# Optimization experiments

Hardware: AMD Instinct MI355X
Metric: run time of the kernel (lower is better)

The kernel has to match this reference:

```python
import jax, jax.numpy as jnp
import numpy as np
import math

D_MODEL = 1024
NUM_HEADS = 16
D_K = D_MODEL // NUM_HEADS
SEQ_LEN = 2048
THETA = 10000.0


def _rope_tables(seq_len, d_k, theta):
    # inv_freq over even dims, angles repeated-interleaved to full d_k
    inv_freq = theta ** (-jnp.arange(0, d_k, 2, dtype=jnp.float32) / d_k)  # [d_k/2]
    pos = jnp.arange(seq_len, dtype=jnp.float32)                          # [s]
    angles = pos[:, None] * inv_freq[None, :]                             # [s, d_k/2]
    angles = jnp.repeat(angles, 2, axis=-1)                               # [s, d_k]
    return jnp.cos(angles), jnp.sin(angles)


def _rotate_half(x):
    # interleaved pairs: (x0,x1,x2,x3,...) -> (-x1,x0,-x3,x2,...)
    x_even = x[..., ::2]
    x_odd = x[..., 1::2]
    return jnp.stack([-x_odd, x_even], axis=-1).reshape(x.shape)


def _apply_rope(x, cos, sin):
    # x: [b, h, s, d_k]; cos/sin: [s, d_k]
    return x * cos + _rotate_half(x) * sin


def setup_inputs() -> dict:
    key = jax.random.key(0)
    ks = jax.random.split(key, 5)
    scale = 1.0 / math.sqrt(D_MODEL)
    X = jax.random.normal(ks[0], (2, SEQ_LEN, D_MODEL), dtype=jnp.float32)
    Wq = jax.random.normal(ks[1], (D_MODEL, D_MODEL), dtype=jnp.float32) * scale
    Wk = jax.random.normal(ks[2], (D_MODEL, D_MODEL), dtype=jnp.float32) * scale
    Wv = jax.random.normal(ks[3], (D_MODEL, D_MODEL), dtype=jnp.float32) * scale
    Wo = jax.random.normal(ks[4], (D_MODEL, D_MODEL), dtype=jnp.float32) * scale
    return {"X": X, "Wq": Wq, "Wk": Wk, "Wv": Wv, "Wo": Wo}


def reference(X, Wq, Wk, Wv, Wo):
    b, s, _ = X.shape
    h, dk = NUM_HEADS, D_K

    def proj(W):
        return (X @ W.T).reshape(b, s, h, dk).transpose(0, 2, 1, 3)  # [b,h,s,dk]

    q, k, v = proj(Wq), proj(Wk), proj(Wv)

    cos, sin = _rope_tables(s, dk, THETA)
    q = _apply_rope(q, cos, sin)
    k = _apply_rope(k, cos, sin)

    scores = jnp.einsum('bhid,bhjd->bhij', q, k) / math.sqrt(dk)
    causal = jnp.tril(jnp.ones((s, s), dtype=bool))
    scores = jnp.where(causal[None, None], scores, -jnp.inf)
    probs = jax.nn.softmax(scores, axis=-1)
    attended = jnp.einsum('bhij,bhjd->bhid', probs, v)               # [b,h,s,dk]

    out = attended.transpose(0, 2, 1, 3).reshape(b, s, h * dk)
    return out @ Wo.T
```

## Files before the change

kernel.cpp:

```cpp
#include <hip/hip_runtime.h>
#include <stdint.h>

#define D_MODEL 1024
#define NUM_HEADS 16
#define DK 64
#define SEQ 2048
#define BATCH 2
#define MROWS (BATCH * SEQ)
#define LOG2E 1.4426950408889634f
#define FIXM 14.0f

typedef short bf16x8 __attribute__((ext_vector_type(8)));
typedef float f32x4 __attribute__((ext_vector_type(4)));

__device__ __forceinline__ unsigned short f2bf(float f) {
    unsigned int u = __float_as_uint(f);
    u = (u + 0x7fffu + ((u >> 16) & 1u)) >> 16;
    return (unsigned short)u;
}
__device__ __forceinline__ unsigned short f2bf_trunc(float f) {
    return (unsigned short)(__float_as_uint(f) >> 16);
}
__device__ __forceinline__ float bf2f(unsigned short h) {
    return __uint_as_float(((unsigned int)h) << 16);
}
__device__ __forceinline__ void async16(const void* g, void* l) {
    __builtin_amdgcn_global_load_lds(
        (const __attribute__((address_space(1))) void*)g,
        (__attribute__((address_space(3))) void*)l, 16, 0, 0);
}
#define SWZ64(row, b) ((((row) * 8) + ((b) ^ ((row) & 7))) * 8)

__global__ void cast_all(const float4* __restrict__ X, const float4* __restrict__ Wq,
                         const float4* __restrict__ Wk, const float4* __restrict__ Wv,
                         const float4* __restrict__ Wo, ushort4* __restrict__ Xb,
                         ushort4* __restrict__ Wqkvb, ushort4* __restrict__ Wob) {
    int i = blockIdx.x * blockDim.x + threadIdx.x;
    const float4* src;
    ushort4* dst;
    int off;
    if (i < 1048576) { src = X; dst = Xb; off = i; }
    else if (i < 1310720) { src = Wq; dst = Wqkvb; off = i - 1048576; }
    else if (i < 1572864) { src = Wk; dst = Wqkvb + 262144; off = i - 1310720; }
    else if (i < 1835008) { src = Wv; dst = Wqkvb + 524288; off = i - 1572864; }
    else { src = Wo; dst = Wob; off = i - 1835008; }
    float4 v = src[off];
    ushort4 o;
    o.x = f2bf(v.x); o.y = f2bf(v.y); o.z = f2bf(v.z); o.w = f2bf(v.w);
    dst[off] = o;
}

template <int TN, int OUT_BF16>
__global__ __launch_bounds__(256) void gemm_tile(
    const unsigned short* __restrict__ A, const unsigned short* __restrict__ B,
    void* __restrict__ Cout, int M, int N, int K) {
    __shared__ unsigned short As[128 * 64];
    __shared__ unsigned short Bs[TN * 64];
    const int m0 = blockIdx.y * 128, n0 = blockIdx.x * TN;
    const int t = threadIdx.x;
    const int lane = t & 63, wave = t >> 6;
    const int mA = lane & 15, quad = lane >> 4;
    constexpr int MI = (TN == 128) ? 4 : 2;
    constexpr int NI = 4;
    const int wr = (TN == 128) ? (wave >> 1) * 64 : wave * 32;
    const int wc = (TN == 128) ? (wave & 1) * 64 : 0;

    f32x4 acc[MI][NI] = {};
    for (int k0 = 0; k0 < K; k0 += 64) {
#pragma unroll
        for (int i = 0; i < 4; ++i) {
            int ch = i * 256 + t;
            int r = ch >> 3, b = (ch & 7) ^ (r & 7);
            async16(A + (size_t)(m0 + r) * K + k0 + b * 8, (char*)As + ch * 16);
        }
#pragma unroll
        for (int i = 0; i < TN / 32; ++i) {
            int ch = i * 256 + t;
            int r = ch >> 3, b = (ch & 7) ^ (r & 7);
            async16(B + (size_t)(n0 + r) * K + k0 + b * 8, (char*)Bs + ch * 16);
        }
        __syncthreads();
#pragma unroll
        for (int kk = 0; kk < 2; ++kk) {
            bf16x8 af[MI], bfr[NI];
#pragma unroll
            for (int mi = 0; mi < MI; ++mi) {
                int rr = wr + mi * 16 + mA;
                af[mi] = *(const bf16x8*)&As[SWZ64(rr, kk * 4 + quad)];
            }
#pragma unroll
            for (int ni = 0; ni < NI; ++ni) {
                int rr = wc + ni * 16 + mA;
                bfr[ni] = *(const bf16x8*)&Bs[SWZ64(rr, kk * 4 + quad)];
            }
#pragma unroll
            for (int mi = 0; mi < MI; ++mi)
#pragma unroll
                for (int ni = 0; ni < NI; ++ni)
                    acc[mi][ni] = __builtin_amdgcn_mfma_f32_16x16x32_bf16(
                        af[mi], bfr[ni], acc[mi][ni], 0, 0, 0);
        }
        __syncthreads();
    }
#pragma unroll
    for (int mi = 0; mi < MI; ++mi)
#pragma unroll
        for (int ni = 0; ni < NI; ++ni)
#pragma unroll
            for (int r = 0; r < 4; ++r) {
                int gm = m0 + wr + mi * 16 + quad * 4 + r;
                int gn = n0 + wc + ni * 16 + mA;
                if (OUT_BF16)
                    ((unsigned short*)Cout)[(size_t)gm * N + gn] = f2bf(acc[mi][ni][r]);
                else
                    ((float*)Cout)[(size_t)gm * N + gn] = acc[mi][ni][r];
            }
}

__global__ __launch_bounds__(256) void rope_vt(const unsigned short* __restrict__ QKV,
                                               unsigned short* __restrict__ Qr,
                                               unsigned short* __restrict__ Kr,
                                               unsigned short* __restrict__ Vt) {
    __shared__ unsigned short T[64][80];
    const int bx = blockIdx.x;
    const int t = threadIdx.x;
    if (bx < 4096) {
        int tid = bx * 256 + t;
        int bs = tid >> 8;
        int p4 = tid & 255;
        int b = bs >> 11, spos = bs & 2047;
        int h = p4 >> 4, dd = (p4 & 15) * 4;
        float sn0, cs0, sn1, cs1;
        {
            float if0 = __expf(-(float)dd * (9.210340371976184f / 64.0f));
            float if1 = __expf(-(float)(dd + 2) * (9.210340371976184f / 64.0f));
            __sincosf((float)spos * if0, &sn0, &cs0);
            __sincosf((float)spos * if1, &sn1, &cs1);
        }
        size_t src = (size_t)bs * 3072 + h * 64 + dd;
        ushort4 qw = *(const ushort4*)&QKV[src];
        ushort4 kw = *(const ushort4*)&QKV[src + 1024];
        ushort4 qo_, ko_;
        float e = bf2f(qw.x), o = bf2f(qw.y);
        qo_.x = f2bf(e * cs0 - o * sn0); qo_.y = f2bf(o * cs0 + e * sn0);
        e = bf2f(qw.z); o = bf2f(qw.w);
        qo_.z = f2bf(e * cs1 - o * sn1); qo_.w = f2bf(o * cs1 + e * sn1);
        e = bf2f(kw.x); o = bf2f(kw.y);
        ko_.x = f2bf(e * cs0 - o * sn0); ko_.y = f2bf(o * cs0 + e * sn0);
        e = bf2f(kw.z); o = bf2f(kw.w);
        ko_.z = f2bf(e * cs1 - o * sn1); ko_.w = f2bf(o * cs1 + e * sn1);
        size_t qb = (((size_t)(b * NUM_HEADS + h) * SEQ + spos) * DK + dd);
        *(ushort4*)&Qr[qb] = qo_;
        *(ushort4*)&Kr[qb] = ko_;
    } else {
        int idx = bx - 4096;
        const int s0 = (idx & 31) * 64, bh = idx >> 5;
        const int b = bh >> 4, h = bh & 15;
#pragma unroll
        for (int i = 0; i < 2; ++i) {
            int ch = i * 256 + t;
            int row = ch >> 3, bc = ch & 7;
            *(int4*)&T[row][bc * 8] =
                *(const int4*)&QKV[(size_t)(b * SEQ + s0 + row) * 3072 + 2048 + h * 64 + bc * 8];
        }
        __syncthreads();
#pragma unroll
        for (int i = 0; i < 2; ++i) {
            int ch = i * 256 + t;
            int d = ch >> 3, sb = ch & 7;
            unsigned short tmp[8];
#pragma unroll
            for (int j = 0; j < 8; ++j) tmp[j] = T[sb * 8 + j][d];
            *(int4*)&Vt[(size_t)bh * DK * SEQ + (size_t)d * SEQ + s0 + sb * 8] = *(int4*)tmp;
        }
    }
}

__global__ __launch_bounds__(256, 4) void flash_attn6(
    const unsigned short* __restrict__ Qr, const unsigned short* __restrict__ Kr,
    const unsigned short* __restrict__ Vt, unsigned short* __restrict__ Att) {
    __shared__ unsigned short Ks[2][64 * 64];
    __shared__ unsigned short Vs[2][64 * 64];
    __shared__ unsigned short Ps[4][16 * 64];
    const int bh = blockIdx.x;
    const int qt = 31 - (int)blockIdx.y;
    const int t = threadIdx.x;
    const int lane = t & 63, wave = t >> 6;
    const int mA = lane & 15, quad = lane >> 4;
    const int qr0 = qt * 64 + wave * 16;
    const size_t qkbase = (size_t)bh * SEQ * DK;
    const unsigned short* Kg = Kr + qkbase;
    const unsigned short* Vg = Vt + (size_t)bh * DK * SEQ;

    bf16x8 aq[2];
#pragma unroll
    for (int c = 0; c < 2; ++c) {
        bf16x8 raw = *(const bf16x8*)&Qr[qkbase + (size_t)(qr0 + mA) * DK + c * 32 + quad * 8];
        bf16x8 s;
#pragma unroll
        for (int j = 0; j < 8; ++j)
            s[j] = (short)f2bf(bf2f((unsigned short)raw[j]) * (0.125f * LOG2E));
        aq[c] = s;
    }

    f32x4 accT[4] = {};
    float lsum[4] = {};

#pragma unroll
    for (int i = 0; i < 2; ++i) {
        int ch = i * 256 + t;
        int row = ch >> 3, sb = (ch & 7) ^ (row & 7);
        async16(Kg + (size_t)row * DK + sb * 8, (char*)Ks[0] + ch * 16);
        async16(Vg + (size_t)row * SEQ + sb * 8, (char*)Vs[0] + ch * 16);
    }

    for (int jt = 0; jt <= qt; ++jt) {
        __syncthreads();
        const int cur = jt & 1;
        if (jt < qt) {
            const int j1 = (jt + 1) * 64;
#pragma unroll
            for (int i = 0; i < 2; ++i) {
                int ch = i * 256 + t;
                int row = ch >> 3, sb = (ch & 7) ^ (row & 7);
                async16(Kg + (size_t)(j1 + row) * DK + sb * 8, (char*)Ks[cur ^ 1] + ch * 16);
                async16(Vg + (size_t)row * SEQ + j1 + sb * 8, (char*)Vs[cur ^ 1] + ch * 16);
            }
        }
        const int j0 = jt * 64;
        const unsigned short* Kt = Ks[cur];
        const unsigned short* Vtile = Vs[cur];
        unsigned short* Pw = Ps[wave];

        f32x4 sc[4] = {};
#pragma unroll
        for (int js = 0; js < 4; ++js) {
            int row = js * 16 + mA;
            bf16x8 b0 = *(const bf16x8*)&Kt[SWZ64(row, quad)];
            bf16x8 b1 = *(const bf16x8*)&Kt[SWZ64(row, quad + 4)];
            sc[js] = __builtin_amdgcn_mfma_f32_16x16x32_bf16(aq[0], b0, sc[js], 0, 0, 0);
            sc[js] = __builtin_amdgcn_mfma_f32_16x16x32_bf16(aq[1], b1, sc[js], 0, 0, 0);
        }
        if (jt == qt) {
#pragma unroll
            for (int js = 0; js < 4; ++js) {
                int gcol = j0 + js * 16 + mA;
#pragma unroll
                for (int r = 0; r < 4; ++r)
                    if (gcol > qr0 + quad * 4 + r) sc[js][r] = -1e30f;
            }
        }

#pragma unroll
        for (int js = 0; js < 4; ++js)
#pragma unroll
            for (int r = 0; r < 4; ++r) {
                float p = __builtin_amdgcn_exp2f(sc[js][r] - FIXM);
                lsum[r] += p;
                int q = quad * 4 + r;
                Pw[SWZ64(q, js * 2 + (mA >> 3)) + (mA & 7)] = f2bf_trunc(p);
            }
        bf16x8 ap0 = *(const bf16x8*)&Pw[SWZ64(mA, quad)];
        bf16x8 ap1 = *(const bf16x8*)&Pw[SWZ64(mA, quad + 4)];
#pragma unroll
        for (int tn = 0; tn < 4; ++tn) {
            int row = tn * 16 + mA;
            bf16x8 bv0 = *(const bf16x8*)&Vtile[SWZ64(row, quad)];
            bf16x8 bv1 = *(const bf16x8*)&Vtile[SWZ64(row, quad + 4)];
            accT[tn] = __builtin_amdgcn_mfma_f32_16x16x32_bf16(bv0, ap0, accT[tn], 0, 0, 0);
            accT[tn] = __builtin_amdgcn_mfma_f32_16x16x32_bf16(bv1, ap1, accT[tn], 0, 0, 0);
        }
    }

#pragma unroll
    for (int r = 0; r < 4; ++r)
#pragma unroll
        for (int off = 1; off < 16; off <<= 1)
            lsum[r] += __shfl_xor(lsum[r], off, 64);
    __syncthreads();
    float* LL = (float*)Ks;
    if (mA == 0)
#pragma unroll
        for (int r = 0; r < 4; ++r) LL[wave * 16 + quad * 4 + r] = lsum[r];
    __syncthreads();
    const float rl = 1.0f / LL[wave * 16 + mA];

    const int b = bh >> 4, h = bh & 15;
#pragma unroll
    for (int tn = 0; tn < 4; ++tn) {
        ushort4 o;
        o.x = f2bf(accT[tn][0] * rl);
        o.y = f2bf(accT[tn][1] * rl);
        o.z = f2bf(accT[tn][2] * rl);
        o.w = f2bf(accT[tn][3] * rl);
        *(ushort4*)&Att[(size_t)(b * SEQ + qr0 + mA) * D_MODEL + h * DK + tn * 16 + quad * 4] = o;
    }
}

extern "C" void kernel_launch(void* const* d_in, const int* in_sizes, int n_in,
                              void* d_out, int out_size, void* d_ws, size_t ws_size,
                              hipStream_t stream) {
    const float* X = (const float*)d_in[0];
    const float* Wq = (const float*)d_in[1];
    const float* Wk = (const float*)d_in[2];
    const float* Wv = (const float*)d_in[3];
    const float* Wo = (const float*)d_in[4];

    char* ws = (char*)d_ws;
    unsigned short* Xb     = (unsigned short*)(ws + 0);
    unsigned short* Wqkvb  = (unsigned short*)(ws + (8u << 20));
    unsigned short* Wob    = (unsigned short*)(ws + (14u << 20));
    unsigned short* QKVraw = (unsigned short*)(ws + (16u << 20));
    unsigned short* Kr     = (unsigned short*)(ws + (40u << 20));
    unsigned short* Vt     = (unsigned short*)(ws + (48u << 20));
    unsigned short* Qr     = Xb;
    unsigned short* Att    = QKVraw;

    cast_all<<<8192, 256, 0, stream>>>((const float4*)X, (const float4*)Wq,
                                       (const float4*)Wk, (const float4*)Wv,
                                       (const float4*)Wo, (ushort4*)Xb,
                                       (ushort4*)Wqkvb, (ushort4*)Wob);

    gemm_tile<128, 1><<<dim3(3072 / 128, MROWS / 128), 256, 0, stream>>>(
        Xb, Wqkvb, QKVraw, MROWS, 3072, D_MODEL);

    rope_vt<<<4096 + 1024, 256, 0, stream>>>(QKVraw, Qr, Kr, Vt);

    flash_attn6<<<dim3(BATCH * NUM_HEADS, 32), 256, 0, stream>>>(Qr, Kr, Vt, Att);

    gemm_tile<64, 0><<<dim3(D_MODEL / 64, MROWS / 128), 256, 0, stream>>>(
        Att, Wob, d_out, MROWS, D_MODEL, D_MODEL);
}
```

Measured before the change: 183.0 us.

## Use 32x32 MFMA with 128-row query tiles in flash attention

The attention kernel now processes 128 query rows per block (32 per wave) using 32x32x16 bf16 MFMAs instead of 16x16x32, halving the grid and doubling reuse of each K/V tile loaded into LDS. Waves whose rows are entirely before a key tile skip it, and setprio is raised around MFMA bursts. The trade-off is more registers (launch bounds drop to 2 blocks per CU), a larger P buffer, and fewer blocks, which can hurt load balance across the causal triangle.

```diff
diff --git a/kernel.cpp b/kernel.cpp
--- a/kernel.cpp
+++ b/kernel.cpp
@@ -12,6 +12,7 @@
 
 typedef short bf16x8 __attribute__((ext_vector_type(8)));
 typedef float f32x4 __attribute__((ext_vector_type(4)));
+typedef float f32x16 __attribute__((ext_vector_type(16)));
 
 __device__ __forceinline__ unsigned short f2bf(float f) {
     unsigned int u = __float_as_uint(f);
@@ -176,35 +177,42 @@
     }
 }
 
-__global__ __launch_bounds__(256, 4) void flash_attn6(
+__global__ __launch_bounds__(256, 2) void flash_attn7(
     const unsigned short* __restrict__ Qr, const unsigned short* __restrict__ Kr,
     const unsigned short* __restrict__ Vt, unsigned short* __restrict__ Att) {
     __shared__ unsigned short Ks[2][64 * 64];
     __shared__ unsigned short Vs[2][64 * 64];
-    __shared__ unsigned short Ps[4][16 * 64];
+    __shared__ unsigned short Ps[4][32 * 64];
     const int bh = blockIdx.x;
-    const int qt = 31 - (int)blockIdx.y;
+    const int qt = 15 - (int)blockIdx.y;
     const int t = threadIdx.x;
     const int lane = t & 63, wave = t >> 6;
-    const int mA = lane & 15, quad = lane >> 4;
-    const int qr0 = qt * 64 + wave * 16;
+    const int l31 = lane & 31, lh = lane >> 5;
+    const int qb = qt * 128 + wave * 32;
     const size_t qkbase = (size_t)bh * SEQ * DK;
     const unsigned short* Kg = Kr + qkbase;
     const unsigned short* Vg = Vt + (size_t)bh * DK * SEQ;
-
-    bf16x8 aq[2];
-#pragma unroll
-    for (int c = 0; c < 2; ++c) {
-        bf16x8 raw = *(const bf16x8*)&Qr[qkbase + (size_t)(qr0 + mA) * DK + c * 32 + quad * 8];
+    const int jtmax = 2 * qt + 1;
+
+    bf16x8 aq[4];
+#pragma unroll
+    for (int kk = 0; kk < 4; ++kk) {
+        bf16x8 raw = *(const bf16x8*)&Qr[qkbase + (size_t)(qb + l31) * DK + kk * 16 + lh * 8];
         bf16x8 s;
 #pragma unroll
         for (int j = 0; j < 8; ++j)
             s[j] = (short)f2bf(bf2f((unsigned short)raw[j]) * (0.125f * LOG2E));
-        aq[c] = s;
-    }
-
-    f32x4 accT[4] = {};
-    float lsum[4] = {};
+        aq[kk] = s;
+    }
+
+    f32x16 accT[2];
+#pragma unroll
+    for (int ti = 0; ti < 2; ++ti)
+#pragma unroll
+        for (int r = 0; r < 16; ++r) accT[ti][r] = 0.f;
+    float lsum[16];
+#pragma unroll
+    for (int r = 0; r < 16; ++r) lsum[r] = 0.f;
 
 #pragma unroll
     for (int i = 0; i < 2; ++i) {
@@ -214,10 +222,11 @@
         async16(Vg + (size_t)row * SEQ + sb * 8, (char*)Vs[0] + ch * 16);
     }
 
-    for (int jt = 0; jt <= qt; ++jt) {
+    unsigned short* Pw = Ps[wave];
+    for (int jt = 0; jt <= jtmax; ++jt) {
         __syncthreads();
         const int cur = jt & 1;
-        if (jt < qt) {
+        if (jt < jtmax) {
             const int j1 = (jt + 1) * 64;
 #pragma unroll
             for (int i = 0; i < 2; ++i) {
@@ -228,73 +237,82 @@
             }
         }
         const int j0 = jt * 64;
+        if (j0 > qb + 31) continue;
         const unsigned short* Kt = Ks[cur];
         const unsigned short* Vtile = Vs[cur];
-        unsigned short* Pw = Ps[wave];
-
-        f32x4 sc[4] = {};
-#pragma unroll
-        for (int js = 0; js < 4; ++js) {
-            int row = js * 16 + mA;
-            bf16x8 b0 = *(const bf16x8*)&Kt[SWZ64(row, quad)];
-            bf16x8 b1 = *(const bf16x8*)&Kt[SWZ64(row, quad + 4)];
-            sc[js] = __builtin_amdgcn_mfma_f32_16x16x32_bf16(aq[0], b0, sc[js], 0, 0, 0);
-            sc[js] = __builtin_amdgcn_mfma_f32_16x16x32_bf16(aq[1], b1, sc[js], 0, 0, 0);
-        }
-        if (jt == qt) {
-#pragma unroll
-            for (int js = 0; js < 4; ++js) {
-                int gcol = j0 + js * 16 + mA;
-#pragma unroll
-                for (int r = 0; r < 4; ++r)
-                    if (gcol > qr0 + quad * 4 + r) sc[js][r] = -1e30f;
-            }
-        }
-
-#pragma unroll
-        for (int js = 0; js < 4; ++js)
-#pragma unroll
-            for (int r = 0; r < 4; ++r) {
-                float p = __builtin_amdgcn_exp2f(sc[js][r] - FIXM);
+        const bool straddle = (j0 + 63 > qb);
+
+#pragma unroll
+        for (int ni = 0; ni < 2; ++ni) {
+            f32x16 sc;
+#pragma unroll
+            for (int r = 0; r < 16; ++r) sc[r] = 0.f;
+            __builtin_amdgcn_s_setprio(1);
+#pragma unroll
+            for (int kk = 0; kk < 4; ++kk) {
+                bf16x8 kf = *(const bf16x8*)&Kt[SWZ64(ni * 32 + l31, kk * 2 + lh)];
+                sc = __builtin_amdgcn_mfma_f32_32x32x16_bf16(aq[kk], kf, sc, 0, 0, 0);
+            }
+            __builtin_amdgcn_s_setprio(0);
+            const int jg = j0 + ni * 32 + l31;
+            if (straddle) {
+#pragma unroll
+                for (int r = 0; r < 16; ++r) {
+                    int ql = (r & 3) + 8 * (r >> 2) + 4 * lh;
+                    if (jg > qb + ql) sc[r] = -1e30f;
+                }
+            }
+#pragma unroll
+            for (int r = 0; r < 16; ++r) {
+                float p = __builtin_amdgcn_exp2f(sc[r] - FIXM);
                 lsum[r] += p;
-                int q = quad * 4 + r;
-                Pw[SWZ64(q, js * 2 + (mA >> 3)) + (mA & 7)] = f2bf_trunc(p);
-            }
-        bf16x8 ap0 = *(const bf16x8*)&Pw[SWZ64(mA, quad)];
-        bf16x8 ap1 = *(const bf16x8*)&Pw[SWZ64(mA, quad + 4)];
-#pragma unroll
-        for (int tn = 0; tn < 4; ++tn) {
-            int row = tn * 16 + mA;
-            bf16x8 bv0 = *(const bf16x8*)&Vtile[SWZ64(row, quad)];
-            bf16x8 bv1 = *(const bf16x8*)&Vtile[SWZ64(row, quad + 4)];
-            accT[tn] = __builtin_amdgcn_mfma_f32_16x16x32_bf16(bv0, ap0, accT[tn], 0, 0, 0);
-            accT[tn] = __builtin_amdgcn_mfma_f32_16x16x32_bf16(bv1, ap1, accT[tn], 0, 0, 0);
-        }
-    }
-
-#pragma unroll
-    for (int r = 0; r < 4; ++r)
-#pragma unroll
-        for (int off = 1; off < 16; off <<= 1)
+                int ql = (r & 3) + 8 * (r >> 2) + 4 * lh;
+                Pw[SWZ64(ql, ni * 4 + (l31 >> 3)) + (lane & 7)] = f2bf_trunc(p);
+            }
+        }
+
+        bf16x8 ap[4];
+#pragma unroll
+        for (int kk = 0; kk < 4; ++kk)
+            ap[kk] = *(const bf16x8*)&Pw[SWZ64(l31, kk * 2 + lh)];
+        __builtin_amdgcn_s_setprio(1);
+#pragma unroll
+        for (int ti = 0; ti < 2; ++ti)
+#pragma unroll
+            for (int kk = 0; kk < 4; ++kk) {
+                bf16x8 vf = *(const bf16x8*)&Vtile[SWZ64(ti * 32 + l31, kk * 2 + lh)];
+                accT[ti] = __builtin_amdgcn_mfma_f32_32x32x16_bf16(vf, ap[kk], accT[ti], 0, 0, 0);
+            }
+        __builtin_amdgcn_s_setprio(0);
+    }
+
+#pragma unroll
+    for (int r = 0; r < 16; ++r)
+#pragma unroll
+        for (int off = 1; off < 32; off <<= 1)
             lsum[r] += __shfl_xor(lsum[r], off, 64);
     __syncthreads();
     float* LL = (float*)Ks;
-    if (mA == 0)
-#pragma unroll
-        for (int r = 0; r < 4; ++r) LL[wave * 16 + quad * 4 + r] = lsum[r];
+    if (l31 == 0)
+#pragma unroll
+        for (int r = 0; r < 16; ++r)
+            LL[wave * 32 + (r & 3) + 8 * (r >> 2) + 4 * lh] = lsum[r];
     __syncthreads();
-    const float rl = 1.0f / LL[wave * 16 + mA];
+    const float rl = 1.0f / LL[wave * 32 + l31];
 
     const int b = bh >> 4, h = bh & 15;
-#pragma unroll
-    for (int tn = 0; tn < 4; ++tn) {
-        ushort4 o;
-        o.x = f2bf(accT[tn][0] * rl);
-        o.y = f2bf(accT[tn][1] * rl);
-        o.z = f2bf(accT[tn][2] * rl);
-        o.w = f2bf(accT[tn][3] * rl);
-        *(ushort4*)&Att[(size_t)(b * SEQ + qr0 + mA) * D_MODEL + h * DK + tn * 16 + quad * 4] = o;
-    }
+    const int qg = qb + l31;
+#pragma unroll
+    for (int ti = 0; ti < 2; ++ti)
+#pragma unroll
+        for (int rg = 0; rg < 4; ++rg) {
+            ushort4 o;
+            o.x = f2bf(accT[ti][rg * 4 + 0] * rl);
+            o.y = f2bf(accT[ti][rg * 4 + 1] * rl);
+            o.z = f2bf(accT[ti][rg * 4 + 2] * rl);
+            o.w = f2bf(accT[ti][rg * 4 + 3] * rl);
+            *(ushort4*)&Att[(size_t)(b * SEQ + qg) * D_MODEL + h * DK + ti * 32 + 8 * rg + 4 * lh] = o;
+        }
 }
 
 extern "C" void kernel_launch(void* const* d_in, const int* in_sizes, int n_in,
@@ -326,7 +344,7 @@
 
     rope_vt<<<4096 + 1024, 256, 0, stream>>>(QKVraw, Qr, Kr, Vt);
 
-    flash_attn6<<<dim3(BATCH * NUM_HEADS, 32), 256, 0, stream>>>(Qr, Kr, Vt, Att);
+    flash_attn7<<<dim3(BATCH * NUM_HEADS, 16), 256, 0, stream>>>(Qr, Kr, Vt, Att);
 
     gemm_tile<64, 0><<<dim3(D_MODEL / 64, MROWS / 128), 256, 0, stream>>>(
         Att, Wob, d_out, MROWS, D_MODEL, D_MODEL);
```

New measurement: 190.0 us. 1.04x slower.
